# Performance work log

Measured on AMD Instinct MI355X. Metric: run time of the kernel, lower is better.

## Reference

```python
import math
import jax, jax.numpy as jnp
import numpy as np

HEADS = 8
DIM_HEAD = 64
N_WIN = 6


def setup_inputs() -> dict:
    key = jax.random.key(0)
    ks = jax.random.split(key, 5)
    b, N, D = 1, 12288, 512
    inner = HEADS * DIM_HEAD  # 512
    x = jax.random.normal(ks[0], (b, N, D), dtype=jnp.float32)
    s = 1.0 / math.sqrt(D)
    Wq = jax.random.normal(ks[1], (inner, D), dtype=jnp.float32) * s
    Wk = jax.random.normal(ks[2], (inner, D), dtype=jnp.float32) * s
    Wv = jax.random.normal(ks[3], (inner, D), dtype=jnp.float32) * s
    Wo = jax.random.normal(ks[4], (D, inner), dtype=jnp.float32) * s
    bo = jnp.zeros((D,), dtype=jnp.float32)
    return {"x": x, "Wq": Wq, "Wk": Wk, "Wv": Wv, "Wo": Wo, "bo": bo}


def reference(x, Wq, Wk, Wv, Wo, bo):
    b, N, D = x.shape
    H = int(math.sqrt(N // 12))  # feature map is H x 12H
    W = N // H                   # 12H
    Ww = W // N_WIN              # window width 2H
    L = H * Ww                   # tokens per window

    # projections (torch Linear: y = x @ W^T)
    q = x @ Wq.T
    k = x @ Wk.T
    v = x @ Wv.T

    def to_windows(t):
        # [b, (H W), inner] -> [b, nwin, L, heads, dim_head]; tokens within a
        # window keep (h w) row-major order, matching the torch rearranges.
        t = t.reshape(b, H, N_WIN, Ww, HEADS, DIM_HEAD)
        return t.transpose(0, 2, 1, 3, 4, 5).reshape(b, N_WIN, L, HEADS, DIM_HEAD)

    qw, kw, vw = to_windows(q), to_windows(k), to_windows(v)

    scale = 1.0 / math.sqrt(DIM_HEAD)
    scores = jnp.einsum('bgqhd,bgkhd->bghqk', qw, kw) * scale  # [b,6,h,L,L]
    attn = jax.nn.softmax(scores, axis=-1)
    out = jnp.einsum('bghqk,bgkhd->bgqhd', attn, vw)           # [b,6,L,h,d]

    # windows -> full map -> tokens
    out = out.reshape(b, N_WIN, H, Ww, HEADS * DIM_HEAD)
    out = out.transpose(0, 2, 1, 3, 4).reshape(b, N, HEADS * DIM_HEAD)
    return out @ Wo.T + bo
```

## Files before the change

kernel.cpp:

```cpp
#include <hip/hip_runtime.h>
#include <hip/hip_bf16.h>

typedef __bf16 bf16_t;
typedef __attribute__((ext_vector_type(8))) __bf16 bf16x8;
typedef __attribute__((ext_vector_type(4))) __bf16 bf16x4;
typedef __attribute__((ext_vector_type(4))) float f32x4;

#define MFMA16(a, b, c) __builtin_amdgcn_mfma_f32_16x16x32_bf16((a), (b), (c), 0, 0, 0)
#define EXP2F(x) __builtin_amdgcn_exp2f(x)

#define NTOK 12288
#define DMODEL 512
#define LWIN 2048
#define NGH 48
#define LOG2E 1.44269504088896340736f

__device__ __forceinline__ void async_copy16(const bf16_t* g, bf16_t* l) {
    __builtin_amdgcn_global_load_lds((const __attribute__((address_space(1))) void*)g,
                                     (__attribute__((address_space(3))) void*)l, 16, 0, 0);
}

__global__ void convert_bf16(const float* __restrict__ x,
                             const float* __restrict__ wq, const float* __restrict__ wk,
                             const float* __restrict__ wv, const float* __restrict__ wo,
                             bf16_t* __restrict__ xbf, bf16_t* __restrict__ wqkv,
                             bf16_t* __restrict__ wob2) {
    const int NX = NTOK * DMODEL;
    const int NW = DMODEL * DMODEL;
    const int total4 = (NX + 4 * NW) >> 2;
    for (int i4 = blockIdx.x * blockDim.x + threadIdx.x; i4 < total4;
         i4 += gridDim.x * blockDim.x) {
        int i = i4 << 2;
        if (i < NX + 3 * NW) {
            const float* src; bf16_t* dst; int off;
            if (i < NX)               { src = x;  dst = xbf;           off = i; }
            else if (i < NX + NW)     { src = wq; dst = wqkv;          off = i - NX; }
            else if (i < NX + 2 * NW) { src = wk; dst = wqkv + NW;     off = i - NX - NW; }
            else                      { src = wv; dst = wqkv + 2 * NW; off = i - NX - 2 * NW; }
            float4 v = *reinterpret_cast<const float4*>(src + off);
            bf16x4 o;
            o[0] = (bf16_t)v.x; o[1] = (bf16_t)v.y; o[2] = (bf16_t)v.z; o[3] = (bf16_t)v.w;
            *reinterpret_cast<bf16x4*>(dst + off) = o;
        } else {
            int off = i - NX - 3 * NW;
            int j = off >> 9, k = off & 511;
            float4 v = *reinterpret_cast<const float4*>(wo + off);
            bf16x4 hi, lo;
            float f[4] = {v.x, v.y, v.z, v.w};
#pragma unroll
            for (int t = 0; t < 4; t++) {
                bf16_t h = (bf16_t)f[t];
                hi[t] = h;
                lo[t] = (bf16_t)(f[t] - (float)h);
            }
            *reinterpret_cast<bf16x4*>(wob2 + (size_t)j * 1024 + k) = hi;
            *reinterpret_cast<bf16x4*>(wob2 + (size_t)j * 1024 + 512 + k) = lo;
        }
    }
}

__global__ __launch_bounds__(256, 2) void gemm_qkv(
    const bf16_t* __restrict__ A, const bf16_t* __restrict__ B,
    bf16_t* __restrict__ qw, bf16_t* __restrict__ kw, bf16_t* __restrict__ vtw) {
    __shared__ __align__(16) bf16_t sA[128 * 64];
    __shared__ __align__(16) bf16_t sB[128 * 64];
    const int tm = blockIdx.x / 12, tn = blockIdx.x % 12;
    const int tid = threadIdx.x;
    const int lane = tid & 63, wid = tid >> 6;
    const int llo = lane & 15, lhi = lane >> 4;
    const int wr = wid >> 1, wc = wid & 1;

    f32x4 acc[4][4];
    const f32x4 zero = {0.f, 0.f, 0.f, 0.f};
#pragma unroll
    for (int i = 0; i < 4; i++)
#pragma unroll
        for (int j = 0; j < 4; j++) acc[i][j] = zero;

    const bf16_t* Ab = A + (size_t)(tm * 128) * DMODEL;
    const bf16_t* Bb = B + (size_t)(tn * 128) * DMODEL;

    for (int k0 = 0; k0 < DMODEL; k0 += 64) {
#pragma unroll
        for (int s = 0; s < 4; s++) {
            int chunk = tid + s * 256;
            int row = chunk >> 3, c8 = chunk & 7;
            int ldsoff = (wid * 64 + s * 256) * 8;
            async_copy16(Ab + (size_t)row * DMODEL + k0 + c8 * 8, sA + ldsoff);
            async_copy16(Bb + (size_t)row * DMODEL + k0 + c8 * 8, sB + ldsoff);
        }
        __syncthreads();
#pragma unroll
        for (int kk = 0; kk < 2; kk++) {
            bf16x8 af[4], bfr[4];
#pragma unroll
            for (int mi = 0; mi < 4; mi++)
                af[mi] = *reinterpret_cast<const bf16x8*>(
                    &sA[(wr * 64 + mi * 16 + llo) * 64 + kk * 32 + lhi * 8]);
#pragma unroll
            for (int ni = 0; ni < 4; ni++)
                bfr[ni] = *reinterpret_cast<const bf16x8*>(
                    &sB[(wc * 64 + ni * 16 + llo) * 64 + kk * 32 + lhi * 8]);
#pragma unroll
            for (int mi = 0; mi < 4; mi++)
#pragma unroll
                for (int ni = 0; ni < 4; ni++)
                    acc[mi][ni] = MFMA16(af[mi], bfr[ni], acc[mi][ni]);
        }
        __syncthreads();
    }

    const int row0 = tm * 128 + wr * 64;
    const int col0 = tn * 128 + wc * 64;
#pragma unroll
    for (int mi = 0; mi < 4; mi++) {
#pragma unroll
        for (int ni = 0; ni < 4; ni++) {
            int j = col0 + ni * 16 + llo;
            int which = j >> 9;
            int head = (j >> 6) & 7;
            int dim = j & 63;
#pragma unroll
            for (int r = 0; r < 4; r++) {
                int n = row0 + mi * 16 + lhi * 4 + r;
                float val = acc[mi][ni][r];
                int hr = n / 384;
                int rem = n - hr * 384;
                int g = rem >> 6, w = rem & 63;
                int l = (hr << 6) + w;
                size_t gh = (size_t)(g * 8 + head);
                if (which == 0)
                    qw[(gh * LWIN + l) * 64 + dim] = (bf16_t)(val * (0.125f * LOG2E));
                else if (which == 1)
                    kw[(gh * LWIN + l) * 64 + dim] = (bf16_t)val;
                else
                    vtw[(gh * 64 + dim) * LWIN + l] = (bf16_t)val;
            }
        }
    }
}

__global__ __launch_bounds__(256, 2) void attn_win(
    const bf16_t* __restrict__ qw, const bf16_t* __restrict__ kw,
    const bf16_t* __restrict__ vtw, float* __restrict__ aout) {
    __shared__ __align__(16) bf16_t sK[2][64 * 64];
    __shared__ __align__(16) bf16_t sV[2][64 * 64];
    __shared__ __align__(16) bf16_t P[4][16][68];

    const int b = blockIdx.x;
    const int xcd = b & 7;
    const int slot = b >> 3;
    const int gh = xcd * 6 + (slot >> 4);
    const int qtile = slot & 15;
    const int g = gh >> 3, h = gh & 7;
    const int tid = threadIdx.x, lane = tid & 63, wid = tid >> 6;
    const int llo = lane & 15, lhi = lane >> 4;

    const bf16_t* Qb = qw + (size_t)gh * LWIN * 64;
    const bf16_t* Kb = kw + (size_t)gh * LWIN * 64;
    const bf16_t* Vb = vtw + (size_t)gh * 64 * LWIN;

    const int q0 = qtile * 128;
    bf16x8 qa[2][2];
#pragma unroll
    for (int qf = 0; qf < 2; qf++)
#pragma unroll
        for (int dk = 0; dk < 2; dk++)
            qa[qf][dk] = *reinterpret_cast<const bf16x8*>(
                &Qb[(size_t)(q0 + qf * 64 + wid * 16 + llo) * 64 + dk * 32 + lhi * 8]);

    f32x4 O[2][4];
    float rs[2][4];
    const f32x4 zero = {0.f, 0.f, 0.f, 0.f};
#pragma unroll
    for (int qf = 0; qf < 2; qf++) {
#pragma unroll
        for (int dc = 0; dc < 4; dc++) O[qf][dc] = zero;
#pragma unroll
        for (int r = 0; r < 4; r++) rs[qf][r] = 0.f;
    }

    auto stage = [&](int buf, int k0) {
#pragma unroll
        for (int s = 0; s < 2; s++) {
            int chunk = tid + s * 256;
            int row = chunk >> 3, c8 = chunk & 7;
            int c8g = c8 ^ (row & 7);
            async_copy16(Kb + (size_t)(k0 + row) * 64 + c8g * 8,
                         &sK[buf][chunk * 8]);
            async_copy16(Vb + (size_t)row * LWIN + k0 + c8g * 8,
                         &sV[buf][chunk * 8]);
        }
    };

    stage(0, 0);
    __syncthreads();

    for (int t = 0; t < 32; t++) {
        const int cur = t & 1;
        if (t < 31) stage(cur ^ 1, (t + 1) * 64);

        bf16x8 bk[4][2];
#pragma unroll
        for (int kc = 0; kc < 4; kc++) {
            int row = kc * 16 + llo;
#pragma unroll
            for (int kk = 0; kk < 2; kk++)
                bk[kc][kk] = *reinterpret_cast<const bf16x8*>(
                    &sK[cur][row * 64 + (((kk * 4 + lhi) ^ (row & 7)) * 8)]);
        }

        bf16x8 pa[2][2];
#pragma unroll
        for (int qf = 0; qf < 2; qf++) {
            f32x4 s4[4];
#pragma unroll
            for (int kc = 0; kc < 4; kc++) {
                f32x4 acc = zero;
                acc = MFMA16(qa[qf][0], bk[kc][0], acc);
                acc = MFMA16(qa[qf][1], bk[kc][1], acc);
                s4[kc] = acc;
            }
#pragma unroll
            for (int kc = 0; kc < 4; kc++)
#pragma unroll
                for (int r = 0; r < 4; r++) {
                    float p = EXP2F(s4[kc][r]);
                    rs[qf][r] += p;
                    P[wid][lhi * 4 + r][kc * 16 + llo] = (bf16_t)p;
                }
#pragma unroll
            for (int ks = 0; ks < 2; ks++)
                pa[qf][ks] = *reinterpret_cast<const bf16x8*>(
                    &P[wid][llo][ks * 32 + lhi * 8]);
        }

#pragma unroll
        for (int dc = 0; dc < 4; dc++) {
            int row = dc * 16 + llo;
            bf16x8 bv0 = *reinterpret_cast<const bf16x8*>(
                &sV[cur][row * 64 + (((0 + lhi) ^ (row & 7)) * 8)]);
            bf16x8 bv1 = *reinterpret_cast<const bf16x8*>(
                &sV[cur][row * 64 + (((4 + lhi) ^ (row & 7)) * 8)]);
#pragma unroll
            for (int qf = 0; qf < 2; qf++) {
                O[qf][dc] = MFMA16(pa[qf][0], bv0, O[qf][dc]);
                O[qf][dc] = MFMA16(pa[qf][1], bv1, O[qf][dc]);
            }
        }
        __syncthreads();
    }

#pragma unroll
    for (int qf = 0; qf < 2; qf++)
#pragma unroll
        for (int r = 0; r < 4; r++) {
            float t = rs[qf][r];
#pragma unroll
            for (int off = 1; off < 16; off <<= 1) t += __shfl_xor(t, off, 64);
            rs[qf][r] = t;
        }
#pragma unroll
    for (int qf = 0; qf < 2; qf++)
#pragma unroll
        for (int dc = 0; dc < 4; dc++)
#pragma unroll
            for (int r = 0; r < 4; r++) {
                int l = q0 + qf * 64 + wid * 16 + lhi * 4 + r;
                int hr = l >> 6, w = l & 63;
                int n = hr * 384 + g * 64 + w;
                aout[(size_t)n * DMODEL + h * 64 + dc * 16 + llo] =
                    O[qf][dc][r] / rs[qf][r];
            }
}

__global__ __launch_bounds__(256, 2) void gemm_out(
    const float* __restrict__ A, const bf16_t* __restrict__ B2,
    const float* __restrict__ bias, float* __restrict__ C) {
    __shared__ __align__(16) bf16_t sA[128 * 64];
    __shared__ __align__(16) bf16_t sB[128 * 64];
    const int tm = blockIdx.x >> 2, tn = blockIdx.x & 3;
    const int tid = threadIdx.x;
    const int lane = tid & 63, wid = tid >> 6;
    const int llo = lane & 15, lhi = lane >> 4;
    const int wr = wid >> 1, wc = wid & 1;

    f32x4 acc[4][4];
    const f32x4 zero = {0.f, 0.f, 0.f, 0.f};
#pragma unroll
    for (int i = 0; i < 4; i++)
#pragma unroll
        for (int j = 0; j < 4; j++) acc[i][j] = zero;

    const float* Ab = A + (size_t)(tm * 128) * DMODEL;
    const bf16_t* Bb = B2 + (size_t)(tn * 128) * 1024;

    for (int k0 = 0; k0 < 1536; k0 += 64) {
        const int kb = k0 >> 9;
        const int ka = k0 & 511;
        const int kB = (kb == 2 ? 512 : 0) + ka;
#pragma unroll
        for (int s = 0; s < 4; s++) {
            int chunk = tid + s * 256;
            int row = chunk >> 3, c8 = chunk & 7;
            const float* ap = Ab + (size_t)row * DMODEL + ka + c8 * 8;
            float4 f0 = *reinterpret_cast<const float4*>(ap);
            float4 f1 = *reinterpret_cast<const float4*>(ap + 4);
            float f[8] = {f0.x, f0.y, f0.z, f0.w, f1.x, f1.y, f1.z, f1.w};
            bf16x8 o;
#pragma unroll
            for (int t = 0; t < 8; t++) {
                bf16_t hv = (bf16_t)f[t];
                o[t] = (kb == 1) ? (bf16_t)(f[t] - (float)hv) : hv;
            }
            *reinterpret_cast<bf16x8*>(&sA[chunk * 8]) = o;
            int ldsoff = (wid * 64 + s * 256) * 8;
            async_copy16(Bb + (size_t)row * 1024 + kB + c8 * 8, sB + ldsoff);
        }
        __syncthreads();
#pragma unroll
        for (int kk = 0; kk < 2; kk++) {
            bf16x8 af[4], bfr[4];
#pragma unroll
            for (int mi = 0; mi < 4; mi++)
                af[mi] = *reinterpret_cast<const bf16x8*>(
                    &sA[(wr * 64 + mi * 16 + llo) * 64 + kk * 32 + lhi * 8]);
#pragma unroll
            for (int ni = 0; ni < 4; ni++)
                bfr[ni] = *reinterpret_cast<const bf16x8*>(
                    &sB[(wc * 64 + ni * 16 + llo) * 64 + kk * 32 + lhi * 8]);
#pragma unroll
            for (int mi = 0; mi < 4; mi++)
#pragma unroll
                for (int ni = 0; ni < 4; ni++)
                    acc[mi][ni] = MFMA16(af[mi], bfr[ni], acc[mi][ni]);
        }
        __syncthreads();
    }

    const int row0 = tm * 128 + wr * 64;
    const int col0 = tn * 128 + wc * 64;
#pragma unroll
    for (int mi = 0; mi < 4; mi++) {
#pragma unroll
        for (int ni = 0; ni < 4; ni++) {
            int j = col0 + ni * 16 + llo;
            float b = bias[j];
#pragma unroll
            for (int r = 0; r < 4; r++) {
                int n = row0 + mi * 16 + lhi * 4 + r;
                C[(size_t)n * DMODEL + j] = acc[mi][ni][r] + b;
            }
        }
    }
}

extern "C" void kernel_launch(void* const* d_in, const int* in_sizes, int n_in,
                              void* d_out, int out_size, void* d_ws, size_t ws_size,
                              hipStream_t stream) {
    const float* x  = (const float*)d_in[0];
    const float* Wq = (const float*)d_in[1];
    const float* Wk = (const float*)d_in[2];
    const float* Wv = (const float*)d_in[3];
    const float* Wo = (const float*)d_in[4];
    const float* bo = (const float*)d_in[5];
    float* out = (float*)d_out;

    const size_t NX = (size_t)NTOK * DMODEL;
    const size_t NW = (size_t)DMODEL * DMODEL;
    bf16_t* xbf   = (bf16_t*)d_ws;
    bf16_t* wqkv  = xbf + NX;
    bf16_t* wob2  = wqkv + 3 * NW;
    bf16_t* qw    = wob2 + 2 * NW;
    bf16_t* kw    = qw + NX;
    bf16_t* vtw   = kw + NX;
    float*  aoutf = (float*)(vtw + NX);

    convert_bf16<<<2048, 256, 0, stream>>>(x, Wq, Wk, Wv, Wo, xbf, wqkv, wob2);

    gemm_qkv<<<96 * 12, 256, 0, stream>>>(xbf, wqkv, qw, kw, vtw);

    attn_win<<<768, 256, 0, stream>>>(qw, kw, vtw, aoutf);

    gemm_out<<<96 * 4, 256, 0, stream>>>(aoutf, wob2, bo, out);
}
```

Baseline: 283.1 us.

## Stage V transpose via LDS, swizzle P tile, emit split-bf16 attention output

The QKV GEMM now transposes V tiles through shared memory so V^T is written with coalesced 16-byte stores instead of scattered 2-byte writes. The attention kernel swizzles its P scratch tile to avoid bank conflicts, raises launch bounds to 4 blocks per CU, adds setprio around the MFMA sections, unrolls the key loop by 2, and multiplies by a reciprocal row sum. Attention output is written as a bf16 hi/lo pair instead of fp32, so the output GEMM can load A with async copies and skip the per-tile conversion. The output GEMM also uses a 128x64 tile to launch twice as many blocks. These changes trade extra LDS traffic and register pressure for cheaper global memory access.

```diff
diff --git a/kernel.cpp b/kernel.cpp
--- a/kernel.cpp
+++ b/kernel.cpp
@@ -62,8 +62,9 @@
 __global__ __launch_bounds__(256, 2) void gemm_qkv(
     const bf16_t* __restrict__ A, const bf16_t* __restrict__ B,
     bf16_t* __restrict__ qw, bf16_t* __restrict__ kw, bf16_t* __restrict__ vtw) {
-    __shared__ __align__(16) bf16_t sA[128 * 64];
-    __shared__ __align__(16) bf16_t sB[128 * 64];
+    __shared__ __align__(16) bf16_t smem[2 * 128 * 64];
+    bf16_t* sA = smem;
+    bf16_t* sB = smem + 128 * 64;
     const int tm = blockIdx.x / 12, tn = blockIdx.x % 12;
     const int tid = threadIdx.x;
     const int lane = tid & 63, wid = tid >> 6;
@@ -85,9 +86,8 @@
         for (int s = 0; s < 4; s++) {
             int chunk = tid + s * 256;
             int row = chunk >> 3, c8 = chunk & 7;
-            int ldsoff = (wid * 64 + s * 256) * 8;
-            async_copy16(Ab + (size_t)row * DMODEL + k0 + c8 * 8, sA + ldsoff);
-            async_copy16(Bb + (size_t)row * DMODEL + k0 + c8 * 8, sB + ldsoff);
+            async_copy16(Ab + (size_t)row * DMODEL + k0 + c8 * 8, sA + chunk * 8);
+            async_copy16(Bb + (size_t)row * DMODEL + k0 + c8 * 8, sB + chunk * 8);
         }
         __syncthreads();
 #pragma unroll
@@ -112,40 +112,73 @@
 
     const int row0 = tm * 128 + wr * 64;
     const int col0 = tn * 128 + wc * 64;
-#pragma unroll
-    for (int mi = 0; mi < 4; mi++) {
-#pragma unroll
-        for (int ni = 0; ni < 4; ni++) {
-            int j = col0 + ni * 16 + llo;
-            int which = j >> 9;
-            int head = (j >> 6) & 7;
-            int dim = j & 63;
-#pragma unroll
-            for (int r = 0; r < 4; r++) {
-                int n = row0 + mi * 16 + lhi * 4 + r;
-                float val = acc[mi][ni][r];
-                int hr = n / 384;
-                int rem = n - hr * 384;
-                int g = rem >> 6, w = rem & 63;
-                int l = (hr << 6) + w;
-                size_t gh = (size_t)(g * 8 + head);
-                if (which == 0)
-                    qw[(gh * LWIN + l) * 64 + dim] = (bf16_t)(val * (0.125f * LOG2E));
-                else if (which == 1)
-                    kw[(gh * LWIN + l) * 64 + dim] = (bf16_t)val;
-                else
-                    vtw[(gh * 64 + dim) * LWIN + l] = (bf16_t)val;
-            }
-        }
-    }
-}
-
-__global__ __launch_bounds__(256, 2) void attn_win(
+    if (tn < 8) {
+#pragma unroll
+        for (int mi = 0; mi < 4; mi++) {
+#pragma unroll
+            for (int ni = 0; ni < 4; ni++) {
+                int j = col0 + ni * 16 + llo;
+                int which = j >> 9;
+                int head = (j >> 6) & 7;
+                int dim = j & 63;
+#pragma unroll
+                for (int r = 0; r < 4; r++) {
+                    int n = row0 + mi * 16 + lhi * 4 + r;
+                    float val = acc[mi][ni][r];
+                    int hr = n / 384;
+                    int rem = n - hr * 384;
+                    int g = rem >> 6, w = rem & 63;
+                    int l = (hr << 6) + w;
+                    size_t gh = (size_t)(g * 8 + head);
+                    if (which == 0)
+                        qw[(gh * LWIN + l) * 64 + dim] = (bf16_t)(val * (0.125f * LOG2E));
+                    else
+                        kw[(gh * LWIN + l) * 64 + dim] = (bf16_t)val;
+                }
+            }
+        }
+    } else {
+        bf16_t* vt = smem;
+#pragma unroll
+        for (int half = 0; half < 2; half++) {
+            if (wr == half) {
+#pragma unroll
+                for (int mi = 0; mi < 4; mi++)
+#pragma unroll
+                    for (int ni = 0; ni < 4; ni++) {
+                        int col_local = wc * 64 + ni * 16 + llo;
+#pragma unroll
+                        for (int r = 0; r < 4; r++) {
+                            int row_local = mi * 16 + lhi * 4 + r;
+                            vt[col_local * 72 + row_local] = (bf16_t)acc[mi][ni][r];
+                        }
+                    }
+            }
+            __syncthreads();
+            int n0 = tm * 128 + half * 64;
+            int hr = n0 / 384;
+            int g = (n0 - hr * 384) >> 6;
+#pragma unroll
+            for (int p = 0; p < 4; p++) {
+                int drow = p * 32 + (tid >> 3);
+                int lch = (tid & 7) * 8;
+                bf16x8 vv = *reinterpret_cast<const bf16x8*>(&vt[drow * 72 + lch]);
+                int jj = (tn - 8) * 128 + drow;
+                int head = jj >> 6, dim = jj & 63;
+                size_t R = (size_t)(g * 8 + head) * 64 + dim;
+                *reinterpret_cast<bf16x8*>(&vtw[R * LWIN + hr * 64 + lch]) = vv;
+            }
+            __syncthreads();
+        }
+    }
+}
+
+__global__ __launch_bounds__(256, 4) void attn_win(
     const bf16_t* __restrict__ qw, const bf16_t* __restrict__ kw,
-    const bf16_t* __restrict__ vtw, float* __restrict__ aout) {
+    const bf16_t* __restrict__ vtw, bf16_t* __restrict__ aout2) {
     __shared__ __align__(16) bf16_t sK[2][64 * 64];
     __shared__ __align__(16) bf16_t sV[2][64 * 64];
-    __shared__ __align__(16) bf16_t P[4][16][68];
+    __shared__ __align__(16) bf16_t P[4][16 * 64];
 
     const int b = blockIdx.x;
     const int xcd = b & 7;
@@ -196,6 +229,7 @@
     stage(0, 0);
     __syncthreads();
 
+#pragma unroll 2
     for (int t = 0; t < 32; t++) {
         const int cur = t & 1;
         if (t < 31) stage(cur ^ 1, (t + 1) * 64);
@@ -214,6 +248,7 @@
 #pragma unroll
         for (int qf = 0; qf < 2; qf++) {
             f32x4 s4[4];
+            __builtin_amdgcn_s_setprio(1);
 #pragma unroll
             for (int kc = 0; kc < 4; kc++) {
                 f32x4 acc = zero;
@@ -221,20 +256,24 @@
                 acc = MFMA16(qa[qf][1], bk[kc][1], acc);
                 s4[kc] = acc;
             }
+            __builtin_amdgcn_s_setprio(0);
 #pragma unroll
             for (int kc = 0; kc < 4; kc++)
 #pragma unroll
                 for (int r = 0; r < 4; r++) {
                     float p = EXP2F(s4[kc][r]);
                     rs[qf][r] += p;
-                    P[wid][lhi * 4 + r][kc * 16 + llo] = (bf16_t)p;
+                    int row = lhi * 4 + r;
+                    int chn = (kc * 2 + (llo >> 3)) ^ (row & 7);
+                    P[wid][row * 64 + chn * 8 + (llo & 7)] = (bf16_t)p;
                 }
 #pragma unroll
             for (int ks = 0; ks < 2; ks++)
                 pa[qf][ks] = *reinterpret_cast<const bf16x8*>(
-                    &P[wid][llo][ks * 32 + lhi * 8]);
-        }
-
+                    &P[wid][llo * 64 + (((ks * 4 + lhi) ^ (llo & 7)) * 8)]);
+        }
+
+        __builtin_amdgcn_s_setprio(1);
 #pragma unroll
         for (int dc = 0; dc < 4; dc++) {
             int row = dc * 16 + llo;
@@ -248,6 +287,7 @@
                 O[qf][dc] = MFMA16(pa[qf][1], bv1, O[qf][dc]);
             }
         }
+        __builtin_amdgcn_s_setprio(0);
         __syncthreads();
     }
 
@@ -258,7 +298,7 @@
             float t = rs[qf][r];
 #pragma unroll
             for (int off = 1; off < 16; off <<= 1) t += __shfl_xor(t, off, 64);
-            rs[qf][r] = t;
+            rs[qf][r] = 1.0f / t;
         }
 #pragma unroll
     for (int qf = 0; qf < 2; qf++)
@@ -269,87 +309,85 @@
                 int l = q0 + qf * 64 + wid * 16 + lhi * 4 + r;
                 int hr = l >> 6, w = l & 63;
                 int n = hr * 384 + g * 64 + w;
-                aout[(size_t)n * DMODEL + h * 64 + dc * 16 + llo] =
-                    O[qf][dc][r] / rs[qf][r];
+                float o = O[qf][dc][r] * rs[qf][r];
+                bf16_t hv = (bf16_t)o;
+                size_t base = (size_t)n * 1024 + h * 64 + dc * 16 + llo;
+                aout2[base] = hv;
+                aout2[base + 512] = (bf16_t)(o - (float)hv);
             }
 }
 
 __global__ __launch_bounds__(256, 2) void gemm_out(
-    const float* __restrict__ A, const bf16_t* __restrict__ B2,
+    const bf16_t* __restrict__ A2, const bf16_t* __restrict__ B2,
     const float* __restrict__ bias, float* __restrict__ C) {
     __shared__ __align__(16) bf16_t sA[128 * 64];
-    __shared__ __align__(16) bf16_t sB[128 * 64];
-    const int tm = blockIdx.x >> 2, tn = blockIdx.x & 3;
+    __shared__ __align__(16) bf16_t sB[64 * 64];
+    const int tm = blockIdx.x >> 3, tn = blockIdx.x & 7;
     const int tid = threadIdx.x;
     const int lane = tid & 63, wid = tid >> 6;
     const int llo = lane & 15, lhi = lane >> 4;
     const int wr = wid >> 1, wc = wid & 1;
 
-    f32x4 acc[4][4];
+    f32x4 acc[4][2];
     const f32x4 zero = {0.f, 0.f, 0.f, 0.f};
 #pragma unroll
     for (int i = 0; i < 4; i++)
 #pragma unroll
-        for (int j = 0; j < 4; j++) acc[i][j] = zero;
-
-    const float* Ab = A + (size_t)(tm * 128) * DMODEL;
-    const bf16_t* Bb = B2 + (size_t)(tn * 128) * 1024;
+        for (int j = 0; j < 2; j++) acc[i][j] = zero;
+
+    const bf16_t* Ab = A2 + (size_t)(tm * 128) * 1024;
+    const bf16_t* Bb = B2 + (size_t)(tn * 64) * 1024;
 
     for (int k0 = 0; k0 < 1536; k0 += 64) {
         const int kb = k0 >> 9;
         const int ka = k0 & 511;
+        const int kA = (kb == 1 ? 512 : 0) + ka;
         const int kB = (kb == 2 ? 512 : 0) + ka;
 #pragma unroll
         for (int s = 0; s < 4; s++) {
             int chunk = tid + s * 256;
             int row = chunk >> 3, c8 = chunk & 7;
-            const float* ap = Ab + (size_t)row * DMODEL + ka + c8 * 8;
-            float4 f0 = *reinterpret_cast<const float4*>(ap);
-            float4 f1 = *reinterpret_cast<const float4*>(ap + 4);
-            float f[8] = {f0.x, f0.y, f0.z, f0.w, f1.x, f1.y, f1.z, f1.w};
-            bf16x8 o;
-#pragma unroll
-            for (int t = 0; t < 8; t++) {
-                bf16_t hv = (bf16_t)f[t];
-                o[t] = (kb == 1) ? (bf16_t)(f[t] - (float)hv) : hv;
-            }
-            *reinterpret_cast<bf16x8*>(&sA[chunk * 8]) = o;
-            int ldsoff = (wid * 64 + s * 256) * 8;
-            async_copy16(Bb + (size_t)row * 1024 + kB + c8 * 8, sB + ldsoff);
+            async_copy16(Ab + (size_t)row * 1024 + kA + c8 * 8, sA + chunk * 8);
+        }
+#pragma unroll
+        for (int s = 0; s < 2; s++) {
+            int chunk = tid + s * 256;
+            int row = chunk >> 3, c8 = chunk & 7;
+            async_copy16(Bb + (size_t)row * 1024 + kB + c8 * 8, sB + chunk * 8);
         }
         __syncthreads();
 #pragma unroll
         for (int kk = 0; kk < 2; kk++) {
-            bf16x8 af[4], bfr[4];
+            bf16x8 af[4], bfr[2];
 #pragma unroll
             for (int mi = 0; mi < 4; mi++)
                 af[mi] = *reinterpret_cast<const bf16x8*>(
                     &sA[(wr * 64 + mi * 16 + llo) * 64 + kk * 32 + lhi * 8]);
 #pragma unroll
-            for (int ni = 0; ni < 4; ni++)
+            for (int ni = 0; ni < 2; ni++)
                 bfr[ni] = *reinterpret_cast<const bf16x8*>(
-                    &sB[(wc * 64 + ni * 16 + llo) * 64 + kk * 32 + lhi * 8]);
+                    &sB[(wc * 32 + ni * 16 + llo) * 64 + kk * 32 + lhi * 8]);
 #pragma unroll
             for (int mi = 0; mi < 4; mi++)
 #pragma unroll
-                for (int ni = 0; ni < 4; ni++)
+                for (int ni = 0; ni < 2; ni++)
                     acc[mi][ni] = MFMA16(af[mi], bfr[ni], acc[mi][ni]);
         }
         __syncthreads();
     }
 
     const int row0 = tm * 128 + wr * 64;
-    const int col0 = tn * 128 + wc * 64;
+    const int col0 = tn * 64 + wc * 32;
 #pragma unroll
     for (int mi = 0; mi < 4; mi++) {
 #pragma unroll
-        for (int ni = 0; ni < 4; ni++) {
+        for (int ni = 0; ni < 2; ni++) {
             int j = col0 + ni * 16 + llo;
-            float b = bias[j];
+            float bv = bias[j];
 #pragma unroll
             for (int r = 0; r < 4; r++) {
                 int n = row0 + mi * 16 + lhi * 4 + r;
-                C[(size_t)n * DMODEL + j] = acc[mi][ni][r] + b;
+                C[(size_t)n * DMODEL + j] = acc[mi][ni][r] + bv;
             }
         }
     }
@@ -374,13 +412,13 @@
     bf16_t* qw    = wob2 + 2 * NW;
     bf16_t* kw    = qw + NX;
     bf16_t* vtw   = kw + NX;
-    float*  aoutf = (float*)(vtw + NX);
+    bf16_t* aout2 = vtw + NX;
 
     convert_bf16<<<2048, 256, 0, stream>>>(x, Wq, Wk, Wv, Wo, xbf, wqkv, wob2);
 
     gemm_qkv<<<96 * 12, 256, 0, stream>>>(xbf, wqkv, qw, kw, vtw);
 
-    attn_win<<<768, 256, 0, stream>>>(qw, kw, vtw, aoutf);
-
-    gemm_out<<<96 * 4, 256, 0, stream>>>(aoutf, wob2, bo, out);
-}
+    attn_win<<<768, 256, 0, stream>>>(qw, kw, vtw, aout2);
+
+    gemm_out<<<96 * 8, 256, 0, stream>>>(aout2, wob2, bo, out);
+}
```

Result: slower. 353.6 us (+24.9%).
